# Kernel tuning notes

Measured on AMD Instinct MI355X. Metric: run time of the kernel, lower is better.

Reference implementation:

```python
import jax, jax.numpy as jnp
import numpy as np

E = 1024
H = 16
HD = E // H  # head_dim = 64
N, T, S = 2, 2048, 2048
NEG = -1e9


def setup_inputs() -> dict:
    key = jax.random.key(0)
    ks = jax.random.split(key, 12)
    s = 0.02
    inp = {
        "query": jax.random.normal(ks[0], (N, T, E), jnp.float32),
        "key": jax.random.normal(ks[1], (N, S, E), jnp.float32),
        "value": jax.random.normal(ks[2], (N, S, E), jnp.float32),
        # causal mask: mask[i, j] == 0 means target i cannot attend to source j
        "attn_mask": jnp.tril(jnp.ones((T, S), jnp.float32)),
        "pad_mask": jnp.zeros((N, S), bool),
        "Wq": jax.random.normal(ks[3], (E, E), jnp.float32) * s,
        "bq": jnp.zeros((E,), jnp.float32),
        "Wk": jax.random.normal(ks[4], (E, E), jnp.float32) * s,
        "bk": jnp.zeros((E,), jnp.float32),
        "Wv": jax.random.normal(ks[5], (E, E), jnp.float32) * s,
        "bv": jnp.zeros((E,), jnp.float32),
        "Wp": jax.random.normal(ks[6], (E, E), jnp.float32) * s,
        "bp": jnp.zeros((E,), jnp.float32),
    }
    return inp


def reference(query, key, value, attn_mask, pad_mask, Wq, bq, Wk, bk, Wv, bv, Wp, bp):
    n, t, _ = query.shape
    _, srcl, _ = key.shape
    # Linear projections (torch Linear: x @ W.T + b), split into heads
    Q = (query @ Wq.T + bq).reshape(n, t, H, HD).transpose(0, 2, 1, 3)      # (N,H,T,HD)
    K = (key @ Wk.T + bk).reshape(n, srcl, H, HD).transpose(0, 2, 1, 3)     # (N,H,S,HD)
    V = (value @ Wv.T + bv).reshape(n, srcl, H, HD).transpose(0, 2, 1, 3)   # (N,H,S,HD)
    scores = jnp.einsum("nhtd,nhsd->nhts", Q, K) / jnp.sqrt(jnp.float32(HD))
    scores = jnp.where(pad_mask[:, None, None, :], NEG, scores)
    scores = jnp.where(attn_mask[None, None, :, :] == 0, NEG, scores)
    att = jax.nn.softmax(scores, axis=-1)  # dropout=0 (eval)
    Y = jnp.einsum("nhts,nhsd->nhtd", att, V)
    Y = Y.transpose(0, 2, 1, 3).reshape(n, t, E)
    return Y @ Wp.T + bp
```

## Files before the change

### kernel.cpp

```cpp
#include <hip/hip_runtime.h>
#include <hip/hip_bf16.h>

#define E_  1024
#define H_  16
#define HD_ 64
#define NB  2
#define T_  2048
#define S_  2048
#define KD  1024

typedef __attribute__((ext_vector_type(8))) short short8;
typedef __attribute__((ext_vector_type(4))) short short4v;
typedef __attribute__((ext_vector_type(4))) float floatx4;

static __device__ __forceinline__ unsigned short f2bf(float f) {
    unsigned int u = __float_as_uint(f);
    unsigned int r = (u + 0x7FFFu + ((u >> 16) & 1u)) >> 16;
    return (unsigned short)r;
}

static __device__ __forceinline__ floatx4 mfma16(short8 a, short8 b, floatx4 c) {
    return __builtin_amdgcn_mfma_f32_16x16x32_bf16(a, b, c, 0, 0, 0);
}

static __device__ __forceinline__ void gload_lds16(const void* g, void* l) {
    __builtin_amdgcn_global_load_lds(
        (const __attribute__((address_space(1))) unsigned int*)g,
        (__attribute__((address_space(3))) unsigned int*)l, 16, 0, 0);
}

__global__ __launch_bounds__(256) void conv_all_kernel(
    const float* __restrict__ wq, const float* __restrict__ wk,
    const float* __restrict__ wv, const float* __restrict__ wp,
    const float* __restrict__ qi, const float* __restrict__ ki,
    const float* __restrict__ vi,
    unsigned short* __restrict__ Wb, unsigned short* __restrict__ Xb)
{
    const int NW4 = 1 << 18;
    const int NX4 = 1 << 20;
    const int TOT = 4 * NW4 + 3 * NX4;
    int idx = blockIdx.x * 256 + threadIdx.x;
    for (int i4 = idx; i4 < TOT; i4 += 262144) {
        const float* s; unsigned short* d; int off4;
        if (i4 < 4 * NW4) {
            int seg = i4 >> 18; off4 = i4 & (NW4 - 1);
            s = (seg == 0) ? wq : (seg == 1) ? wk : (seg == 2) ? wv : wp;
            d = Wb + ((size_t)seg << 20);
        } else {
            int j = i4 - 4 * NW4; int seg = j >> 20; off4 = j & (NX4 - 1);
            s = (seg == 0) ? qi : (seg == 1) ? ki : vi;
            d = Xb + ((size_t)seg << 22);
        }
        float4 v = *(const float4*)&s[(size_t)off4 * 4];
        short4v b;
        b[0] = (short)f2bf(v.x); b[1] = (short)f2bf(v.y);
        b[2] = (short)f2bf(v.z); b[3] = (short)f2bf(v.w);
        *(short4v*)&d[(size_t)off4 * 4] = b;
    }
}

__global__ __launch_bounds__(256) void proj_qkv_kernel(
    const unsigned short* __restrict__ Xb, const unsigned short* __restrict__ Wb,
    const float* __restrict__ bq, const float* __restrict__ bk, const float* __restrict__ bv,
    unsigned short* __restrict__ Qh, unsigned short* __restrict__ K2, unsigned short* __restrict__ V2)
{
    const int z = blockIdx.z;
    const unsigned short* X = Xb + ((size_t)z << 22);
    const unsigned short* W = Wb + ((size_t)z << 20);
    const float* bias = (z == 0) ? bq : (z == 1) ? bk : bv;
    unsigned short* dst = (z == 0) ? Qh : (z == 1) ? K2 : V2;

    __shared__ unsigned short Sm[16384];
    unsigned short* As = Sm;
    unsigned short* Bs = Sm + 8192;

    const int tid  = threadIdx.x;
    const int lane = tid & 63;
    const int w    = tid >> 6;
    const int wm   = w >> 1, wn = w & 1;
    const int m0   = blockIdx.x * 128;
    const int e0   = blockIdx.y * 128;
    const int l15  = lane & 15, lg = lane >> 4;

    floatx4 acc[4][4];
#pragma unroll
    for (int mi = 0; mi < 4; ++mi)
#pragma unroll
        for (int ni = 0; ni < 4; ++ni)
            acc[mi][ni] = (floatx4){0.f, 0.f, 0.f, 0.f};

    const int rc = lane >> 3;
    const int sl = (lane & 7) ^ rc;

    for (int kt = 0; kt < KD / 64; ++kt) {
        const int k0 = kt * 64;
#pragma unroll
        for (int jj = 0; jj < 4; ++jj) {
            int c = w * 4 + jj;
            int row = c * 8 + rc;
            gload_lds16(&X[(size_t)(m0 + row) * KD + k0 + sl * 8], &As[c * 512]);
            gload_lds16(&W[(size_t)(e0 + row) * KD + k0 + sl * 8], &Bs[c * 512]);
        }
        __syncthreads();

#pragma unroll
        for (int ks = 0; ks < 2; ++ks) {
            short8 af[4], bf[4];
#pragma unroll
            for (int mi = 0; mi < 4; ++mi) {
                int r_ = wm * 64 + mi * 16 + l15;
                af[mi] = *(const short8*)&As[r_ * 64 + (((ks * 4 + lg) ^ (r_ & 7)) << 3)];
            }
#pragma unroll
            for (int ni = 0; ni < 4; ++ni) {
                int r_ = wn * 64 + ni * 16 + l15;
                bf[ni] = *(const short8*)&Bs[r_ * 64 + (((ks * 4 + lg) ^ (r_ & 7)) << 3)];
            }
#pragma unroll
            for (int mi = 0; mi < 4; ++mi)
#pragma unroll
                for (int ni = 0; ni < 4; ++ni)
                    acc[mi][ni] = mfma16(af[mi], bf[ni], acc[mi][ni]);
        }
        __syncthreads();
    }

    if (z != 2) {
#pragma unroll
        for (int mi = 0; mi < 4; ++mi)
#pragma unroll
            for (int ni = 0; ni < 4; ++ni) {
                int col = wn * 64 + ni * 16 + l15;
                float bb = bias[e0 + col];
#pragma unroll
                for (int r = 0; r < 4; ++r) {
                    int row = wm * 64 + mi * 16 + (lg << 2) + r;
                    Sm[row * 128 + (col ^ ((row & 7) << 3))] =
                        f2bf(acc[mi][ni][r] + bb);
                }
            }
    } else {
#pragma unroll
        for (int mi = 0; mi < 4; ++mi)
#pragma unroll
            for (int ni = 0; ni < 4; ++ni) {
                int col = wn * 64 + ni * 16 + l15;
                float bb = bias[e0 + col];
                int rb = wm * 64 + mi * 16 + (lg << 2);
                short4v sv;
#pragma unroll
                for (int r = 0; r < 4; ++r) sv[r] = (short)f2bf(acc[mi][ni][r] + bb);
                *(short4v*)&Sm[col * 128 + (rb ^ ((col & 7) << 3))] = sv;
            }
    }
    __syncthreads();

    {
        const int r0 = tid >> 1;
        const int cb = (tid & 1) * 64;
#pragma unroll
        for (int j = 0; j < 8; ++j) {
            int c = cb + j * 8;
            short8 v = *(const short8*)&Sm[r0 * 128 + (c ^ ((r0 & 7) << 3))];
            if (z == 0) {
                int m = m0 + r0, nn = m >> 11, t = m & (T_ - 1);
                int e = e0 + c, hh = e >> 6, d = e & 63;
                size_t hb = (size_t)(nn * H_ + hh) * (T_ * HD_);
                *(short8*)&dst[hb + (size_t)t * HD_ + d] = v;
            } else if (z == 1) {
                int m = m0 + r0, nn = m >> 11, t = m & (T_ - 1);
                int e = e0 + c, hh = e >> 6, d = e & 63;
                size_t hb = (size_t)(nn * H_ + hh) * (T_ * HD_);
                *(short8*)&dst[hb + (t >> 6) * 4096 + (t & 63) * 64 +
                               (((d >> 3) ^ (t & 7)) << 3)] = v;
            } else {
                int e = e0 + r0, hh = e >> 6, d = e & 63;
                int m = m0 + c, nn = m >> 11, t = m & (T_ - 1);
                size_t hb = (size_t)(nn * H_ + hh) * (T_ * HD_);
                *(short8*)&dst[hb + (t >> 6) * 4096 + d * 64 +
                               ((((t >> 3) & 7) ^ (d & 7)) << 3)] = v;
            }
        }
    }
}

__global__ __launch_bounds__(256) void flash_attn_kernel(
    const unsigned short* __restrict__ Qh, const unsigned short* __restrict__ K2,
    const unsigned short* __restrict__ V2, unsigned short* __restrict__ Y)
{
    const int linear = blockIdx.x;
    const int nid = (linear & 7) * 64 + (linear >> 3);
    const int pb = nid & 15, h = (nid >> 4) & 15, n = nid >> 8;

    const int tid = threadIdx.x, lane = tid & 63, w = tid >> 6;
    const int l15 = lane & 15, lg = lane >> 4;

    const unsigned short* Qp = Qh + (size_t)(n * H_ + h) * (T_ * HD_);
    const unsigned short* Kt = K2 + (size_t)(n * H_ + h) * (T_ * HD_);
    const unsigned short* Vt = V2 + (size_t)(n * H_ + h) * (T_ * HD_);

    __shared__ unsigned short Ks_l[4096];
    __shared__ unsigned short VT_l[4096];
    __shared__ unsigned short Ps[64][72];

    const int prow = w * 16 + lg * 4;
    const int arow = w * 16 + l15;
    const int sw7  = l15 & 7;

#pragma unroll
    for (int side = 0; side < 2; ++side) {
        const int qt = side ? (31 - pb) : pb;
        const int q0 = qt * 64;

        short8 qf[2];
#pragma unroll
        for (int ks = 0; ks < 2; ++ks)
            qf[ks] = *(const short8*)&Qp[(size_t)(q0 + arow) * HD_ + ks * 32 + lg * 8];

        floatx4 o[4];
        float lacc[4];
#pragma unroll
        for (int hi = 0; hi < 4; ++hi) o[hi] = (floatx4){0.f, 0.f, 0.f, 0.f};
#pragma unroll
        for (int r = 0; r < 4; ++r) lacc[r] = 0.f;

        for (int kb = 0; kb <= qt; ++kb) {
            __syncthreads();
            const unsigned short* Ksrc = Kt + kb * 4096;
            const unsigned short* Vsrc = Vt + kb * 4096;
#pragma unroll
            for (int j = 0; j < 2; ++j) {
                int c = w * 2 + j;
                gload_lds16(&Ksrc[c * 512 + lane * 8], &Ks_l[c * 512]);
                gload_lds16(&Vsrc[c * 512 + lane * 8], &VT_l[c * 512]);
            }
            __syncthreads();

            floatx4 sa[4];
#pragma unroll
            for (int ni = 0; ni < 4; ++ni) sa[ni] = (floatx4){0.f, 0.f, 0.f, 0.f};
            __builtin_amdgcn_s_setprio(1);
#pragma unroll
            for (int ks = 0; ks < 2; ++ks) {
                short8 kf[4];
#pragma unroll
                for (int ni = 0; ni < 4; ++ni)
                    kf[ni] = *(const short8*)
                        &Ks_l[(ni * 16 + l15) * 64 + (((ks * 4 + lg) ^ sw7) << 3)];
#pragma unroll
                for (int ni = 0; ni < 4; ++ni)
                    sa[ni] = mfma16(qf[ks], kf[ni], sa[ni]);
            }
            __builtin_amdgcn_s_setprio(0);

            const bool diag = (kb == qt);
            float pv[4][4];
#pragma unroll
            for (int ni = 0; ni < 4; ++ni)
#pragma unroll
                for (int r = 0; r < 4; ++r) {
                    float e = __expf(sa[ni][r] * 0.125f);
                    if (diag && (ni * 16 + l15 > prow + r)) e = 0.f;
                    pv[ni][r] = e;
                }
#pragma unroll
            for (int r = 0; r < 4; ++r)
                lacc[r] += (pv[0][r] + pv[1][r]) + (pv[2][r] + pv[3][r]);

#pragma unroll
            for (int ni = 0; ni < 4; ++ni)
#pragma unroll
                for (int r = 0; r < 4; ++r)
                    Ps[prow + r][(ni * 16 + l15) ^ (lg << 3)] = f2bf(pv[ni][r]);

            __builtin_amdgcn_s_setprio(1);
#pragma unroll
            for (int ks = 0; ks < 2; ++ks) {
                short8 pa = *(const short8*)
                    &Ps[arow][(ks * 32 + lg * 8) ^ ((l15 >> 2) << 3)];
                short8 vt[4];
#pragma unroll
                for (int hi = 0; hi < 4; ++hi)
                    vt[hi] = *(const short8*)
                        &VT_l[(hi * 16 + l15) * 64 + (((ks * 4 + lg) ^ sw7) << 3)];
#pragma unroll
                for (int hi = 0; hi < 4; ++hi)
                    o[hi] = mfma16(pa, vt[hi], o[hi]);
            }
            __builtin_amdgcn_s_setprio(0);
        }

        float linv[4];
#pragma unroll
        for (int r = 0; r < 4; ++r) {
            float l = lacc[r];
#pragma unroll
            for (int off = 1; off < 16; off <<= 1)
                l += __shfl_xor(l, off);
            linv[r] = 1.0f / l;
        }

#pragma unroll
        for (int hi = 0; hi < 4; ++hi) {
            int col = hi * 16 + l15;
#pragma unroll
            for (int r = 0; r < 4; ++r) {
                int t = q0 + prow + r;
                Y[((size_t)n * T_ + t) * E_ + h * HD_ + col] =
                    f2bf(o[hi][r] * linv[r]);
            }
        }
    }
}

__global__ __launch_bounds__(256) void proj_out_kernel(
    const unsigned short* __restrict__ Yb, const unsigned short* __restrict__ Wpb,
    const float* __restrict__ bp, float* __restrict__ out)
{
    __shared__ unsigned char SmB[65536];
    unsigned short* As = (unsigned short*)SmB;
    unsigned short* Bs = As + 8192;
    float* Cf = (float*)SmB;

    const int tid  = threadIdx.x;
    const int lane = tid & 63;
    const int w    = tid >> 6;
    const int wm   = w >> 1, wn = w & 1;
    const int m0   = blockIdx.x * 128;
    const int e0   = blockIdx.y * 128;
    const int l15  = lane & 15, lg = lane >> 4;

    floatx4 acc[4][4];
#pragma unroll
    for (int mi = 0; mi < 4; ++mi)
#pragma unroll
        for (int ni = 0; ni < 4; ++ni)
            acc[mi][ni] = (floatx4){0.f, 0.f, 0.f, 0.f};

    const int rc = lane >> 3;
    const int sl = (lane & 7) ^ rc;

    for (int kt = 0; kt < E_ / 64; ++kt) {
        const int k0 = kt * 64;
#pragma unroll
        for (int jj = 0; jj < 4; ++jj) {
            int c = w * 4 + jj;
            int row = c * 8 + rc;
            gload_lds16(&Yb[(size_t)(m0 + row) * E_ + k0 + sl * 8], &As[c * 512]);
            gload_lds16(&Wpb[(size_t)(e0 + row) * E_ + k0 + sl * 8], &Bs[c * 512]);
        }
        __syncthreads();

#pragma unroll
        for (int ks = 0; ks < 2; ++ks) {
            short8 af[4], bf[4];
#pragma unroll
            for (int mi = 0; mi < 4; ++mi) {
                int r_ = wm * 64 + mi * 16 + l15;
                af[mi] = *(const short8*)&As[r_ * 64 + (((ks * 4 + lg) ^ (r_ & 7)) << 3)];
            }
#pragma unroll
            for (int ni = 0; ni < 4; ++ni) {
                int r_ = wn * 64 + ni * 16 + l15;
                bf[ni] = *(const short8*)&Bs[r_ * 64 + (((ks * 4 + lg) ^ (r_ & 7)) << 3)];
            }
#pragma unroll
            for (int mi = 0; mi < 4; ++mi)
#pragma unroll
                for (int ni = 0; ni < 4; ++ni)
                    acc[mi][ni] = mfma16(af[mi], bf[ni], acc[mi][ni]);
        }
        __syncthreads();
    }

#pragma unroll
    for (int mi = 0; mi < 4; ++mi)
#pragma unroll
        for (int ni = 0; ni < 4; ++ni) {
            int col = wn * 64 + ni * 16 + l15;
            float bb = bp[e0 + col];
#pragma unroll
            for (int r = 0; r < 4; ++r) {
                int row = wm * 64 + mi * 16 + (lg << 2) + r;
                Cf[row * 128 + (col ^ ((row & 7) << 2))] = acc[mi][ni][r] + bb;
            }
        }
    __syncthreads();

    {
        const int r0 = tid >> 1;
        const int cb = (tid & 1) * 64;
        const int m  = m0 + r0;
#pragma unroll
        for (int j = 0; j < 16; ++j) {
            int c = cb + j * 4;
            float4 v = *(const float4*)&Cf[r0 * 128 + (c ^ ((r0 & 7) << 2))];
            *(float4*)&out[(size_t)m * E_ + e0 + c] = v;
        }
    }
}

extern "C" void kernel_launch(void* const* d_in, const int* in_sizes, int n_in,
                              void* d_out, int out_size, void* d_ws, size_t ws_size,
                              hipStream_t stream) {
    const float* query = (const float*)d_in[0];
    const float* key_  = (const float*)d_in[1];
    const float* value = (const float*)d_in[2];
    const float* Wq = (const float*)d_in[5];
    const float* bq = (const float*)d_in[6];
    const float* Wk = (const float*)d_in[7];
    const float* bk = (const float*)d_in[8];
    const float* Wv = (const float*)d_in[9];
    const float* bv = (const float*)d_in[10];
    const float* Wp = (const float*)d_in[11];
    const float* bp = (const float*)d_in[12];
    float* out = (float*)d_out;

    const size_t P = (size_t)NB * H_ * T_ * HD_;
    unsigned short* Qh  = (unsigned short*)d_ws;
    unsigned short* K2  = Qh + P;
    unsigned short* V2  = K2 + P;
    unsigned short* Wb  = V2 + P;
    unsigned short* Xb  = Wb + (4u << 20);
    unsigned short* Yb  = Xb;
    unsigned short* Wpb = Wb + (3u << 20);

    conv_all_kernel<<<dim3(1024), 256, 0, stream>>>(
        Wq, Wk, Wv, Wp, query, key_, value, Wb, Xb);
    proj_qkv_kernel<<<dim3(32, 8, 3), 256, 0, stream>>>(
        Xb, Wb, bq, bk, bv, Qh, K2, V2);
    flash_attn_kernel<<<dim3(512), 256, 0, stream>>>(Qh, K2, V2, Yb);
    proj_out_kernel<<<dim3(32, 8), 256, 0, stream>>>(Yb, Wpb, bp, out);
}
```

Before: 133.9 us.

## Double KV tile to 128 keys per iteration and drop LDS-staged output store

The flash attention loop now loads 128-key K/V tiles per iteration instead of 64, roughly halving the number of barrier-synchronized iterations and doubling MFMA work between syncs. The causal mask uses absolute positions so the last half-tile covering future keys is masked to zero, which can waste compute on the diagonal tile. LDS use in the attention kernel roughly doubles, which may reduce occupancy. Separately, the output projection writes results directly from registers instead of staging them through shared memory for coalesced float4 stores, trading store coalescing for one fewer barrier and less LDS.

```diff
diff --git a/kernel.cpp b/kernel.cpp
--- a/kernel.cpp
+++ b/kernel.cpp
@@ -199,9 +199,9 @@
     const unsigned short* Kt = K2 + (size_t)(n * H_ + h) * (T_ * HD_);
     const unsigned short* Vt = V2 + (size_t)(n * H_ + h) * (T_ * HD_);
 
-    __shared__ unsigned short Ks_l[4096];
-    __shared__ unsigned short VT_l[4096];
-    __shared__ unsigned short Ps[64][72];
+    __shared__ unsigned short Ks_l[8192];
+    __shared__ unsigned short VT_l[8192];
+    __shared__ unsigned short Ps[64][136];
 
     const int prow = w * 16 + lg * 4;
     const int arow = w * 16 + l15;
@@ -211,6 +211,7 @@
     for (int side = 0; side < 2; ++side) {
         const int qt = side ? (31 - pb) : pb;
         const int q0 = qt * 64;
+        const int nkv = (qt + 2) >> 1;
 
         short8 qf[2];
 #pragma unroll
@@ -224,65 +225,68 @@
 #pragma unroll
         for (int r = 0; r < 4; ++r) lacc[r] = 0.f;
 
-        for (int kb = 0; kb <= qt; ++kb) {
+        for (int kb2 = 0; kb2 < nkv; ++kb2) {
             __syncthreads();
-            const unsigned short* Ksrc = Kt + kb * 4096;
-            const unsigned short* Vsrc = Vt + kb * 4096;
-#pragma unroll
-            for (int j = 0; j < 2; ++j) {
-                int c = w * 2 + j;
+            const unsigned short* Ksrc = Kt + kb2 * 8192;
+            const unsigned short* Vsrc = Vt + kb2 * 8192;
+#pragma unroll
+            for (int j = 0; j < 4; ++j) {
+                int c = w * 4 + j;
                 gload_lds16(&Ksrc[c * 512 + lane * 8], &Ks_l[c * 512]);
                 gload_lds16(&Vsrc[c * 512 + lane * 8], &VT_l[c * 512]);
             }
             __syncthreads();
 
-            floatx4 sa[4];
-#pragma unroll
-            for (int ni = 0; ni < 4; ++ni) sa[ni] = (floatx4){0.f, 0.f, 0.f, 0.f};
+            floatx4 sa[8];
+#pragma unroll
+            for (int ni = 0; ni < 8; ++ni) sa[ni] = (floatx4){0.f, 0.f, 0.f, 0.f};
             __builtin_amdgcn_s_setprio(1);
 #pragma unroll
             for (int ks = 0; ks < 2; ++ks) {
-                short8 kf[4];
-#pragma unroll
-                for (int ni = 0; ni < 4; ++ni)
+                short8 kf[8];
+#pragma unroll
+                for (int ni = 0; ni < 8; ++ni)
                     kf[ni] = *(const short8*)
                         &Ks_l[(ni * 16 + l15) * 64 + (((ks * 4 + lg) ^ sw7) << 3)];
 #pragma unroll
-                for (int ni = 0; ni < 4; ++ni)
+                for (int ni = 0; ni < 8; ++ni)
                     sa[ni] = mfma16(qf[ks], kf[ni], sa[ni]);
             }
             __builtin_amdgcn_s_setprio(0);
 
-            const bool diag = (kb == qt);
-            float pv[4][4];
-#pragma unroll
-            for (int ni = 0; ni < 4; ++ni)
+            const bool diag = (kb2 == nkv - 1);
+            const int sbase = kb2 * 128;
+            float pv[8][4];
+#pragma unroll
+            for (int ni = 0; ni < 8; ++ni)
 #pragma unroll
                 for (int r = 0; r < 4; ++r) {
                     float e = __expf(sa[ni][r] * 0.125f);
-                    if (diag && (ni * 16 + l15 > prow + r)) e = 0.f;
+                    if (diag && (sbase + ni * 16 + l15 > q0 + prow + r)) e = 0.f;
                     pv[ni][r] = e;
                 }
 #pragma unroll
             for (int r = 0; r < 4; ++r)
-                lacc[r] += (pv[0][r] + pv[1][r]) + (pv[2][r] + pv[3][r]);
-
-#pragma unroll
-            for (int ni = 0; ni < 4; ++ni)
+                lacc[r] += ((pv[0][r] + pv[1][r]) + (pv[2][r] + pv[3][r]))
+                         + ((pv[4][r] + pv[5][r]) + (pv[6][r] + pv[7][r]));
+
+#pragma unroll
+            for (int ni = 0; ni < 8; ++ni)
 #pragma unroll
                 for (int r = 0; r < 4; ++r)
                     Ps[prow + r][(ni * 16 + l15) ^ (lg << 3)] = f2bf(pv[ni][r]);
 
             __builtin_amdgcn_s_setprio(1);
 #pragma unroll
-            for (int ks = 0; ks < 2; ++ks) {
+            for (int ksp = 0; ksp < 4; ++ksp) {
                 short8 pa = *(const short8*)
-                    &Ps[arow][(ks * 32 + lg * 8) ^ ((l15 >> 2) << 3)];
+                    &Ps[arow][(ksp * 32 + lg * 8) ^ ((l15 >> 2) << 3)];
                 short8 vt[4];
 #pragma unroll
                 for (int hi = 0; hi < 4; ++hi)
                     vt[hi] = *(const short8*)
-                        &VT_l[(hi * 16 + l15) * 64 + (((ks * 4 + lg) ^ sw7) << 3)];
+                        &VT_l[(ksp >> 1) * 4096 + (hi * 16 + l15) * 64 +
+                              ((((ksp & 1) * 4 + lg) ^ sw7) << 3)];
 #pragma unroll
                 for (int hi = 0; hi < 4; ++hi)
                     o[hi] = mfma16(pa, vt[hi], o[hi]);
@@ -317,10 +321,8 @@
     const unsigned short* __restrict__ Yb, const unsigned short* __restrict__ Wpb,
     const float* __restrict__ bp, float* __restrict__ out)
 {
-    __shared__ unsigned char SmB[65536];
-    unsigned short* As = (unsigned short*)SmB;
-    unsigned short* Bs = As + 8192;
-    float* Cf = (float*)SmB;
+    __shared__ unsigned short As[128 * 64];
+    __shared__ unsigned short Bs[128 * 64];
 
     const int tid  = threadIdx.x;
     const int lane = tid & 63;
@@ -374,28 +376,16 @@
     }
 
 #pragma unroll
-    for (int mi = 0; mi < 4; ++mi)
+    for (int mi = 0; mi < 4; ++mi) {
 #pragma unroll
         for (int ni = 0; ni < 4; ++ni) {
-            int col = wn * 64 + ni * 16 + l15;
-            float bb = bp[e0 + col];
+            int e = e0 + wn * 64 + ni * 16 + l15;
+            float bb = bp[e];
 #pragma unroll
             for (int r = 0; r < 4; ++r) {
-                int row = wm * 64 + mi * 16 + (lg << 2) + r;
-                Cf[row * 128 + (col ^ ((row & 7) << 2))] = acc[mi][ni][r] + bb;
-            }
-        }
-    __syncthreads();
-
-    {
-        const int r0 = tid >> 1;
-        const int cb = (tid & 1) * 64;
-        const int m  = m0 + r0;
-#pragma unroll
-        for (int j = 0; j < 16; ++j) {
-            int c = cb + j * 4;
-            float4 v = *(const float4*)&Cf[r0 * 128 + (c ^ ((r0 & 7) << 2))];
-            *(float4*)&out[(size_t)m * E_ + e0 + c] = v;
+                int m = m0 + wm * 64 + mi * 16 + (lg << 2) + r;
+                out[(size_t)m * E_ + e] = acc[mi][ni][r] + bb;
+            }
         }
     }
 }
```

Measured after the change: 127.3 us. -5.0%, faster.
